# Kernel tuning notes

Measured on AMD Instinct MI355X. Metric: run time of the kernel, lower is better.

## Reference

```python
import jax, jax.numpy as jnp
import numpy as np

N_NODES = 50000
N_EDGES = 600000
K = 4
BN_EPS = 1e-5


def setup_inputs() -> dict:
    key = jax.random.key(0)
    ks = jax.random.split(key, 8)
    x = jax.random.normal(ks[0], (N_NODES, 128), dtype=jnp.float32)
    edge_index = jax.random.randint(ks[1], (2, N_EDGES), 0, N_NODES, dtype=jnp.int64)
    edge_weight = jax.random.uniform(ks[2], (N_EDGES,), dtype=jnp.float32)
    conv_w = jax.random.normal(ks[3], (10, K, 128, 128), dtype=jnp.float32)
    conv_b = jnp.zeros((10, 128), dtype=jnp.float32)
    bn_gamma = jnp.ones((10, 128), dtype=jnp.float32)
    bn_beta = jnp.zeros((10, 128), dtype=jnp.float32)
    lin_w = jax.random.normal(ks[4], (128, 16), dtype=jnp.float32)
    lin_b = jnp.zeros((16,), dtype=jnp.float32)
    return {"x": x, "edge_index": edge_index, "edge_weight": edge_weight,
            "conv_w": conv_w, "conv_b": conv_b, "bn_gamma": bn_gamma,
            "bn_beta": bn_beta, "lin_w": lin_w, "lin_b": lin_b}


def _cheb_norm(edge_index, edge_weight, n_nodes):
    # PyG ChebConv with lambda_max=2, sym normalization:
    # L_hat = 2L/lambda_max - I = -D^{-1/2} A D^{-1/2}, zero diagonal.
    row, col = edge_index[0], edge_index[1]
    w = jnp.where(row == col, 0.0, edge_weight)  # remove_self_loops
    deg = jax.ops.segment_sum(w, row, num_segments=n_nodes)
    dis = jnp.where(deg > 0, jax.lax.rsqrt(jnp.where(deg > 0, deg, 1.0)), 0.0)
    norm = -dis[row] * w * dis[col]
    return norm


def _propagate(h, norm, src, dst, n_nodes):
    # (L_hat h)[i] = sum over edges (src->dst==i) norm_e * h[src_e]
    return jax.ops.segment_sum(norm[:, None] * h[src], dst, num_segments=n_nodes)


def _cheb_conv(h, norm, src, dst, W, b, n_nodes):
    # W: [K, F_in, F_out]; Chebyshev recurrence T0=h, T1=Lh, Tk=2L T_{k-1} - T_{k-2}
    Tx0 = h
    out = Tx0 @ W[0]
    Tx1 = _propagate(Tx0, norm, src, dst, n_nodes)
    out = out + Tx1 @ W[1]
    for k in range(2, W.shape[0]):
        Tx2 = 2.0 * _propagate(Tx1, norm, src, dst, n_nodes) - Tx0
        out = out + Tx2 @ W[k]
        Tx0, Tx1 = Tx1, Tx2
    return out + b


def _batchnorm(h, gamma, beta):
    mean = jnp.mean(h, axis=0)
    var = jnp.mean(jnp.square(h - mean), axis=0)  # biased, as torch BN
    return gamma * (h - mean) * jax.lax.rsqrt(var + BN_EPS) + beta


def reference(x, edge_index, edge_weight, conv_w, conv_b, bn_gamma, bn_beta, lin_w, lin_b):
    n_nodes = x.shape[0]
    src, dst = edge_index[0], edge_index[1]
    norm = _cheb_norm(edge_index, edge_weight, n_nodes)
    h = x
    for i in range(10):
        h = jax.nn.relu(_cheb_conv(h, norm, src, dst, conv_w[i], conv_b[i], n_nodes))
        h = _batchnorm(h, bn_gamma[i], bn_beta[i])
        # dropout: identity (eval mode / deterministic reference)
    return h @ lin_w + lin_b
```

## Files before the change

### kernel.cpp

```cpp
#include <hip/hip_runtime.h>
#include <hip/hip_bf16.h>
#include <cstddef>

#define NN 50000
#define NE 600000
#define FD 128
#define NL 10
#define BN_EPS 1e-5f
#define NBG ((NN + 127) / 128)
#define SCB ((NN + 255) / 256)

typedef _Float16 f16x8 __attribute__((ext_vector_type(8)));
typedef _Float16 f16x2 __attribute__((ext_vector_type(2)));
typedef float f32x4 __attribute__((ext_vector_type(4)));

__global__ void k_detect(const unsigned int* __restrict__ gamma_raw,
                         const unsigned int* __restrict__ idx_raw,
                         int* __restrict__ flags) {
  if (threadIdx.x == 0 && blockIdx.x == 0) {
    flags[0] = (gamma_raw[0] == 0x3F803F80u) ? 1 : 0;
    int i64 = 1;
    for (int i = 1; i < 64; i += 2)
      if (idx_raw[i] != 0u) i64 = 0;
    flags[1] = i64;
  }
}

__device__ __forceinline__ float ld_f(const void* src, int i, int isbf) {
  if (isbf) {
    unsigned int u = ((const unsigned short*)src)[i];
    return __uint_as_float(u << 16);
  }
  return ((const float*)src)[i];
}

#define R_IDX 1200000
#define R_H   4400000
#define R_EW  5000000
#define R_W   5655360
#define R_P   5661392
__global__ void k_pre(const void* __restrict__ x, const void* __restrict__ eidx,
                      const void* __restrict__ ew, const void* __restrict__ convw,
                      const void* __restrict__ convb, const void* __restrict__ gamma,
                      const void* __restrict__ beta, const void* __restrict__ linw,
                      const void* __restrict__ linb,
                      int* __restrict__ idx32, unsigned int* __restrict__ hbuf,
                      float* __restrict__ ewf, unsigned short* __restrict__ wt,
                      float* __restrict__ convbf, float* __restrict__ gammaf,
                      float* __restrict__ betaf, float* __restrict__ linwf,
                      float* __restrict__ linbf, float* __restrict__ stid,
                      const int* __restrict__ flags) {
  int gid = blockIdx.x * 256 + threadIdx.x;
  int isbf = flags[0];
  if (gid < R_IDX) {
    if (flags[1]) idx32[gid] = (int)((const long long*)eidx)[gid];
    else          idx32[gid] = ((const int*)eidx)[gid];
  } else if (gid < R_H) {
    int i = gid - R_IDX;
    f16x2 p;
    p.x = (_Float16)ld_f(x, i * 2, isbf);
    p.y = (_Float16)ld_f(x, i * 2 + 1, isbf);
    hbuf[i] = *(unsigned int*)&p;
  } else if (gid < R_EW) {
    int i = gid - R_H;
    ewf[i] = ld_f(ew, i, isbf);
  } else if (gid < R_W) {
    int tid = gid - R_EW;
    int L = tid >> 16;
    int r16 = tid & 65535;
    int s = r16 >> 12;
    int r = r16 & 4095;
    int n = r >> 5, kk = r & 31;
    int kc = s >> 2, kb = s & 3;
    int krow = kb * 32 + kk;
    int base = (L * 4) * FD * FD;
    float v;
    if (kc == 0)
      v = ld_f(convw, base + (0 * FD + krow) * FD + n, isbf)
        - ld_f(convw, base + (2 * FD + krow) * FD + n, isbf);
    else if (kc == 1)
      v = ld_f(convw, base + (1 * FD + krow) * FD + n, isbf)
        - 3.f * ld_f(convw, base + (3 * FD + krow) * FD + n, isbf);
    else if (kc == 2)
      v = 2.f * ld_f(convw, base + (2 * FD + krow) * FD + n, isbf);
    else
      v = 4.f * ld_f(convw, base + (3 * FD + krow) * FD + n, isbf);
    _Float16 h = (_Float16)v;
    wt[tid] = *(unsigned short*)&h;
  } else if (gid < R_P) {
    int i = gid - R_W;
    if (i < 1280) convbf[i] = ld_f(convb, i, isbf);
    else if (i < 2560) gammaf[i - 1280] = ld_f(gamma, i - 1280, isbf);
    else if (i < 3840) betaf[i - 2560] = ld_f(beta, i - 2560, isbf);
    else if (i < 5888) linwf[i - 3840] = ld_f(linw, i - 3840, isbf);
    else if (i < 5904) linbf[i - 5888] = ld_f(linb, i - 5888, isbf);
    else { int f = i - 5904; stid[f] = 1.f; stid[128 + f] = 0.f; }
  }
}

__global__ void k_deg(const int* __restrict__ src, const int* __restrict__ dst,
                      const float* __restrict__ w, float* __restrict__ deg,
                      int* __restrict__ counts, int m) {
  int e = blockIdx.x * 256 + threadIdx.x;
  if (e >= m) return;
  int s = src[e], d = dst[e];
  float ww = (s == d) ? 0.f : w[e];
  atomicAdd(&deg[s], ww);
  atomicAdd(&counts[d], 1);
}

__global__ void k_dis(float* __restrict__ deg, int n) {
  int i = blockIdx.x * 256 + threadIdx.x;
  if (i >= n) return;
  float d = deg[i];
  deg[i] = (d > 0.f) ? rsqrtf(d) : 0.f;
}

__global__ void k_scan1(const int* __restrict__ counts, int* __restrict__ bsum, int n) {
  __shared__ int sd[256];
  int i = blockIdx.x * 256 + threadIdx.x;
  sd[threadIdx.x] = (i < n) ? counts[i] : 0;
  __syncthreads();
  for (int off = 128; off; off >>= 1) {
    if (threadIdx.x < off) sd[threadIdx.x] += sd[threadIdx.x + off];
    __syncthreads();
  }
  if (threadIdx.x == 0) bsum[blockIdx.x] = sd[0];
}

__global__ void k_scan2(const int* __restrict__ bsum, int* __restrict__ boff, int nb) {
  __shared__ int sd[256];
  int t = threadIdx.x;
  int v = (t < nb) ? bsum[t] : 0;
  sd[t] = v;
  __syncthreads();
  for (int off = 1; off < 256; off <<= 1) {
    int x = sd[t];
    int add = (t >= off) ? sd[t - off] : 0;
    __syncthreads();
    sd[t] = x + add;
    __syncthreads();
  }
  if (t < nb) boff[t] = sd[t] - v;
}

__global__ void k_scan3(const int* __restrict__ counts, const int* __restrict__ boff,
                        int* __restrict__ rowptr, int* __restrict__ cursor, int n, int m) {
  __shared__ int sd[256];
  int t = threadIdx.x;
  int i = blockIdx.x * 256 + t;
  int v = (i < n) ? counts[i] : 0;
  sd[t] = v;
  __syncthreads();
  for (int off = 1; off < 256; off <<= 1) {
    int x = sd[t];
    int add = (t >= off) ? sd[t - off] : 0;
    __syncthreads();
    sd[t] = x + add;
    __syncthreads();
  }
  if (i < n) {
    int excl = boff[blockIdx.x] + sd[t] - v;
    rowptr[i] = excl;
    cursor[i] = excl;
  }
  if (i == n - 1) rowptr[n] = m;
}

__global__ void k_fill(const int* __restrict__ src, const int* __restrict__ dst,
                       const float* __restrict__ w, const float* __restrict__ dis,
                       int* __restrict__ cursor, int2* __restrict__ esw, int m) {
  int e = blockIdx.x * 256 + threadIdx.x;
  if (e >= m) return;
  int s = src[e], d = dst[e];
  float ww = (s == d) ? 0.f : w[e];
  float nv = -dis[s] * ww * dis[d];
  int pos = atomicAdd(&cursor[d], 1);
  esw[pos] = make_int2(s, __float_as_int(nv));
}

__global__ void k_rowsum(const int* __restrict__ rowptr, const int2* __restrict__ esw,
                         float* __restrict__ rowsum, int n) {
  int node = blockIdx.x * 256 + threadIdx.x;
  if (node >= n) return;
  int beg = rowptr[node], end = rowptr[node + 1];
  float s = 0.f;
  for (int e = beg; e < end; e++) s += __int_as_float(esw[e].y);
  rowsum[node] = s;
}

template <int MODE>
__global__ __launch_bounds__(256) void k_prop(const uint4* __restrict__ h128,
                                              const int* __restrict__ rowptr,
                                              const int2* __restrict__ esw,
                                              const float* __restrict__ st,
                                              const float* __restrict__ rowsum,
                                              uint4* __restrict__ out128, int n) {
  int node = blockIdx.x * 16 + (threadIdx.x >> 4);
  int l = threadIdx.x & 15;
  if (node >= n) return;
  int beg = rowptr[node], end = rowptr[node + 1];
  float a[8];
#pragma unroll
  for (int i = 0; i < 8; i++) a[i] = 0.f;
  for (int e = beg; e < end; e += 8) {
    int   s_[8];
    float w_[8];
#pragma unroll
    for (int j = 0; j < 8; j++) {
      int ee = e + j;
      int ec = (ee < end) ? ee : (end - 1);
      int2 m = esw[ec];
      s_[j] = m.x;
      w_[j] = (ee < end) ? __int_as_float(m.y) : 0.f;
    }
    uint4 g[8];
#pragma unroll
    for (int j = 0; j < 8; j++) g[j] = h128[(size_t)s_[j] * 16 + l];
#pragma unroll
    for (int j = 0; j < 8; j++) {
      f16x2 u0 = *(f16x2*)&g[j].x;
      f16x2 u1 = *(f16x2*)&g[j].y;
      f16x2 u2 = *(f16x2*)&g[j].z;
      f16x2 u3 = *(f16x2*)&g[j].w;
      a[0] = fmaf(w_[j], (float)u0.x, a[0]);
      a[1] = fmaf(w_[j], (float)u0.y, a[1]);
      a[2] = fmaf(w_[j], (float)u1.x, a[2]);
      a[3] = fmaf(w_[j], (float)u1.y, a[3]);
      a[4] = fmaf(w_[j], (float)u2.x, a[4]);
      a[5] = fmaf(w_[j], (float)u2.y, a[5]);
      a[6] = fmaf(w_[j], (float)u3.x, a[6]);
      a[7] = fmaf(w_[j], (float)u3.y, a[7]);
    }
  }
  if (MODE == 0) {
    float4 s0 = *(const float4*)&st[l * 8];
    float4 s1 = *(const float4*)&st[l * 8 + 4];
    float4 t0 = *(const float4*)&st[128 + l * 8];
    float4 t1 = *(const float4*)&st[128 + l * 8 + 4];
    float rs = rowsum[node];
    a[0] = s0.x * a[0] + t0.x * rs;  a[1] = s0.y * a[1] + t0.y * rs;
    a[2] = s0.z * a[2] + t0.z * rs;  a[3] = s0.w * a[3] + t0.w * rs;
    a[4] = s1.x * a[4] + t1.x * rs;  a[5] = s1.y * a[5] + t1.y * rs;
    a[6] = s1.z * a[6] + t1.z * rs;  a[7] = s1.w * a[7] + t1.w * rs;
  }
  f16x2 o0, o1, o2, o3;
  o0.x = (_Float16)a[0]; o0.y = (_Float16)a[1];
  o1.x = (_Float16)a[2]; o1.y = (_Float16)a[3];
  o2.x = (_Float16)a[4]; o2.y = (_Float16)a[5];
  o3.x = (_Float16)a[6]; o3.y = (_Float16)a[7];
  uint4 o;
  o.x = *(unsigned int*)&o0; o.y = *(unsigned int*)&o1;
  o.z = *(unsigned int*)&o2; o.w = *(unsigned int*)&o3;
  out128[(size_t)node * 16 + l] = o;
}

__global__ __launch_bounds__(256) void k_gemm(const unsigned short* __restrict__ T0h,
                                              const unsigned short* __restrict__ T1h,
                                              const unsigned short* __restrict__ T2h,
                                              const unsigned short* __restrict__ T3h,
                                              const unsigned short* __restrict__ Wt,
                                              const float* __restrict__ bias,
                                              const float* __restrict__ st,
                                              unsigned short* __restrict__ outh,
                                              float* __restrict__ stats, int n) {
  __shared__ unsigned short ldsB[2][128 * 40];
  __shared__ float lps[4][128], lqs[4][128];
  int tid = threadIdx.x;
  int wid = tid >> 6, lane = tid & 63;
  int ln = lane & 15, kg = lane >> 4;
  int r0 = blockIdx.x * 128 + wid * 32;

  f32x4 acc[2][8];
#pragma unroll
  for (int rb = 0; rb < 2; rb++)
#pragma unroll
    for (int nb = 0; nb < 8; nb++) acc[rb][nb] = (f32x4){0.f, 0.f, 0.f, 0.f};

  {
    const uint4* g = (const uint4*)(Wt);
    uint4 a = g[tid], b = g[tid + 256];
    *(uint4*)&ldsB[0][(tid >> 2) * 40 + (tid & 3) * 8] = a;
    *(uint4*)&ldsB[0][((tid >> 2) + 64) * 40 + (tid & 3) * 8] = b;
  }
  __syncthreads();

  int rowA0 = r0 + ln;       if (rowA0 >= n) rowA0 = n - 1;
  int rowA1 = r0 + 16 + ln;  if (rowA1 >= n) rowA1 = n - 1;

#pragma unroll
  for (int kc = 0; kc < 4; ++kc) {
    const unsigned short* T = (kc == 0) ? T0h : (kc == 1) ? T1h : (kc == 2) ? T2h : T3h;
#pragma unroll
    for (int kb = 0; kb < 4; ++kb) {
      const int s = kc * 4 + kb;
      const int cur = s & 1;
      uint4 st0, st1;
      if (s < 15) {
        const uint4* g = (const uint4*)(Wt + (s + 1) * 4096);
        st0 = g[tid]; st1 = g[tid + 256];
      }
      f16x8 a0 = *(const f16x8*)(T + (size_t)rowA0 * FD + kb * 32 + kg * 8);
      f16x8 a1 = *(const f16x8*)(T + (size_t)rowA1 * FD + kb * 32 + kg * 8);
      if (kc == 0) {
        const float* sb = st + kb * 32 + kg * 8;
        const float* tb = st + 128 + kb * 32 + kg * 8;
#pragma unroll
        for (int j = 0; j < 8; j++) {
          a0[j] = (_Float16)(sb[j] * (float)a0[j] + tb[j]);
          a1[j] = (_Float16)(sb[j] * (float)a1[j] + tb[j]);
        }
      }
      f16x8 bf[8];
#pragma unroll
      for (int nb = 0; nb < 8; nb++)
        bf[nb] = *(const f16x8*)&ldsB[cur][(nb * 16 + ln) * 40 + kg * 8];
#pragma unroll
      for (int nb = 0; nb < 8; nb++) {
        acc[0][nb] = __builtin_amdgcn_mfma_f32_16x16x32_f16(a0, bf[nb], acc[0][nb], 0, 0, 0);
        acc[1][nb] = __builtin_amdgcn_mfma_f32_16x16x32_f16(a1, bf[nb], acc[1][nb], 0, 0, 0);
      }
      if (s < 15) {
        *(uint4*)&ldsB[cur ^ 1][(tid >> 2) * 40 + (tid & 3) * 8] = st0;
        *(uint4*)&ldsB[cur ^ 1][((tid >> 2) + 64) * 40 + (tid & 3) * 8] = st1;
      }
      __syncthreads();
    }
  }

  float psum[8], psq[8];
#pragma unroll
  for (int nb = 0; nb < 8; nb++) { psum[nb] = 0.f; psq[nb] = 0.f; }
#pragma unroll
  for (int rb = 0; rb < 2; rb++) {
#pragma unroll
    for (int nb = 0; nb < 8; nb++) {
      int col = nb * 16 + ln;
      float bs = bias[col];
#pragma unroll
      for (int r = 0; r < 4; r++) {
        int row = r0 + rb * 16 + kg * 4 + r;
        if (row < n) {
          float v = acc[rb][nb][r] + bs;
          v = fmaxf(v, 0.f);
          _Float16 hv = (_Float16)v;
          outh[(size_t)row * FD + col] = *(unsigned short*)&hv;
          psum[nb] += v;
          psq[nb] += v * v;
        }
      }
    }
  }
#pragma unroll
  for (int nb = 0; nb < 8; nb++) {
    float sv = psum[nb], qv = psq[nb];
    sv += __shfl_xor(sv, 16); sv += __shfl_xor(sv, 32);
    qv += __shfl_xor(qv, 16); qv += __shfl_xor(qv, 32);
    if (kg == 0) { lps[wid][nb * 16 + ln] = sv; lqs[wid][nb * 16 + ln] = qv; }
  }
  __syncthreads();
  if (tid < 128) {
    float sv = lps[0][tid] + lps[1][tid] + lps[2][tid] + lps[3][tid];
    atomicAdd(&stats[tid], sv);
  } else {
    int c = tid - 128;
    float qv = lqs[0][c] + lqs[1][c] + lqs[2][c] + lqs[3][c];
    atomicAdd(&stats[128 + c], qv);
  }
}

__global__ void k_bnfin(const float* __restrict__ stats,
                        const float* __restrict__ gamma, const float* __restrict__ beta,
                        float* __restrict__ st, float invN) {
  int f = threadIdx.x;
  float mean = stats[f] * invN;
  float var = stats[128 + f] * invN - mean * mean;
  float sc = gamma[f] * rsqrtf(var + BN_EPS);
  st[f] = sc;
  st[128 + f] = beta[f] - mean * sc;
}

__global__ void k_final(const unsigned short* __restrict__ h, const float* __restrict__ w,
                        const float* __restrict__ b, const float* __restrict__ st,
                        void* __restrict__ out, int n, const int* __restrict__ flags) {
  __shared__ float lw[2048];
  __shared__ float ls[128], lt[128];
  for (int i = threadIdx.x; i < 2048; i += 256) lw[i] = w[i];
  if (threadIdx.x < 128) { ls[threadIdx.x] = st[threadIdx.x]; lt[threadIdx.x] = st[128 + threadIdx.x]; }
  __syncthreads();
  int node = blockIdx.x * 256 + threadIdx.x;
  if (node >= n) return;
  float acc[16];
#pragma unroll
  for (int c = 0; c < 16; c++) acc[c] = b[c];
  const f16x8* hr = (const f16x8*)(h + (size_t)node * FD);
#pragma unroll 2
  for (int k8 = 0; k8 < 16; k8++) {
    f16x8 hv = hr[k8];
#pragma unroll
    for (int j = 0; j < 8; j++) {
      int f = k8 * 8 + j;
      float x = ls[f] * (float)hv[j] + lt[f];
#pragma unroll
      for (int c = 0; c < 16; c++) acc[c] = fmaf(x, lw[f * 16 + c], acc[c]);
    }
  }
  int isbf = flags[0];
  for (int c = 0; c < 16; c++) {
    int idx = node * 16 + c;
    if (isbf) ((__hip_bfloat16*)out)[idx] = __float2bfloat16(acc[c]);
    else      ((float*)out)[idx] = acc[c];
  }
}

extern "C" void kernel_launch(void* const* d_in, const int* in_sizes, int n_in,
                              void* d_out, int out_size, void* d_ws, size_t ws_size,
                              hipStream_t stream) {
  char* p = (char*)d_ws;
  auto take = [&](size_t bytes) -> void* {
    void* r = (void*)p;
    p += (bytes + 255) & ~size_t(255);
    return r;
  };
  int*   flags  = (int*)  take(64);
  int*   idx32  = (int*)  take(sizeof(int) * 2 * NE);
  float* ewf    = (float*)take(sizeof(float) * NE);
  unsigned short* wtws = (unsigned short*)take(sizeof(short) * NL * 16 * 4096);
  float* convbf = (float*)take(sizeof(float) * NL * FD);
  float* gammaf = (float*)take(sizeof(float) * NL * FD);
  float* betaf  = (float*)take(sizeof(float) * NL * FD);
  float* linwf  = (float*)take(sizeof(float) * FD * 16);
  float* linbf  = (float*)take(sizeof(float) * 16);
  char*  zb     = (char*) take(sizeof(float) * NN + sizeof(int) * NN + sizeof(float) * NL * 256);
  float* deg    = (float*)zb;
  int*   counts = (int*)  (zb + sizeof(float) * NN);
  float* stats  = (float*)(zb + sizeof(float) * NN + sizeof(int) * NN);
  float* rowsum = (float*)take(sizeof(float) * NN);
  int*   rowptr = (int*)  take(sizeof(int) * (NN + 1));
  int*   cursor = (int*)  take(sizeof(int) * NN);
  int*   bsum   = (int*)  take(sizeof(int) * SCB);
  int*   boff   = (int*)  take(sizeof(int) * SCB);
  int2*  esw    = (int2*) take(sizeof(int2) * NE);
  unsigned int* hbuf = (unsigned int*)take(sizeof(int) * (size_t)NN * 64);
  unsigned int* t1   = (unsigned int*)take(sizeof(int) * (size_t)NN * 64);
  unsigned int* t2   = (unsigned int*)take(sizeof(int) * (size_t)NN * 64);
  unsigned int* t3   = (unsigned int*)take(sizeof(int) * (size_t)NN * 64);
  float* stcur  = (float*)take(sizeof(float) * 256);
  float* stid   = (float*)take(sizeof(float) * 256);

  k_detect<<<1, 64, 0, stream>>>((const unsigned int*)d_in[5], (const unsigned int*)d_in[1], flags);

  k_pre<<<(R_P + 255) / 256, 256, 0, stream>>>(d_in[0], d_in[1], d_in[2], d_in[3], d_in[4],
                                               d_in[5], d_in[6], d_in[7], d_in[8],
                                               idx32, hbuf, ewf, wtws,
                                               convbf, gammaf, betaf, linwf, linbf, stid, flags);

  hipMemsetAsync(zb, 0, sizeof(float) * NN + sizeof(int) * NN + sizeof(float) * NL * 256, stream);

  const int* srcI = idx32;
  const int* dstI = idx32 + NE;
  k_deg<<<(NE + 255) / 256, 256, 0, stream>>>(srcI, dstI, ewf, deg, counts, NE);
  k_dis<<<(NN + 255) / 256, 256, 0, stream>>>(deg, NN);
  k_scan1<<<SCB, 256, 0, stream>>>(counts, bsum, NN);
  k_scan2<<<1, 256, 0, stream>>>(bsum, boff, SCB);
  k_scan3<<<SCB, 256, 0, stream>>>(counts, boff, rowptr, cursor, NN, NE);
  k_fill<<<(NE + 255) / 256, 256, 0, stream>>>(srcI, dstI, ewf, deg, cursor, esw, NE);
  k_rowsum<<<(NN + 255) / 256, 256, 0, stream>>>(rowptr, esw, rowsum, NN);

  for (int L = 0; L < NL; ++L) {
    const unsigned short* Wt = wtws + (size_t)L * 16 * 4096;
    const float* stIn = (L == 0) ? stid : stcur;
    k_prop<0><<<(NN + 15) / 16, 256, 0, stream>>>((const uint4*)hbuf, rowptr, esw, stIn, rowsum, (uint4*)t1, NN);
    k_prop<1><<<(NN + 15) / 16, 256, 0, stream>>>((const uint4*)t1, rowptr, esw, nullptr, nullptr, (uint4*)t2, NN);
    k_prop<1><<<(NN + 15) / 16, 256, 0, stream>>>((const uint4*)t2, rowptr, esw, nullptr, nullptr, (uint4*)t3, NN);
    k_gemm<<<NBG, 256, 0, stream>>>((const unsigned short*)hbuf, (const unsigned short*)t1,
                                    (const unsigned short*)t2, (const unsigned short*)t3,
                                    Wt, convbf + L * FD, stIn, (unsigned short*)hbuf, stats + L * 256, NN);
    k_bnfin<<<1, 128, 0, stream>>>(stats + L * 256, gammaf + L * FD, betaf + L * FD, stcur, 1.0f / NN);
  }

  k_final<<<(NN + 255) / 256, 256, 0, stream>>>((const unsigned short*)hbuf, linwf, linbf, stcur, d_out, NN, flags);
}
```

Measured before the change: 1.172 ms.

## Pack edges into 32-bit words, sort nodes by degree bucket, fold BN finalize

Each CSR edge entry shrinks from an int2 to one 32-bit word holding a 16-bit source index and an fp16 normalized weight, halving edge-stream traffic in the propagation kernels. A degree-bucketing pass builds a node order that groups nodes of similar degree so 16-lane groups in a block do similar amounts of gather work. The batch-norm finalize kernel is removed: prop, gemm and final now compute scale and shift from the raw stats in shared memory. The separate rsqrt-degree kernel is fused into the first scan kernel. The cost is reduced precision on edge weights, a 65535-node limit on the packed index, and one extra indirection per node through the order array.

```diff
diff --git a/kernel.cpp b/kernel.cpp
--- a/kernel.cpp
+++ b/kernel.cpp
@@ -9,6 +9,7 @@
 #define BN_EPS 1e-5f
 #define NBG ((NN + 127) / 128)
 #define SCB ((NN + 255) / 256)
+#define NBK 9
 
 typedef _Float16 f16x8 __attribute__((ext_vector_type(8)));
 typedef _Float16 f16x2 __attribute__((ext_vector_type(2)));
@@ -38,7 +39,7 @@
 #define R_H   4400000
 #define R_EW  5000000
 #define R_W   5655360
-#define R_P   5661392
+#define R_P   5661312
 __global__ void k_pre(const void* __restrict__ x, const void* __restrict__ eidx,
                       const void* __restrict__ ew, const void* __restrict__ convw,
                       const void* __restrict__ convb, const void* __restrict__ gamma,
@@ -48,7 +49,7 @@
                       float* __restrict__ ewf, unsigned short* __restrict__ wt,
                       float* __restrict__ convbf, float* __restrict__ gammaf,
                       float* __restrict__ betaf, float* __restrict__ linwf,
-                      float* __restrict__ linbf, float* __restrict__ stid,
+                      float* __restrict__ linbf,
                       const int* __restrict__ flags) {
   int gid = blockIdx.x * 256 + threadIdx.x;
   int isbf = flags[0];
@@ -94,7 +95,6 @@
     else if (i < 3840) betaf[i - 2560] = ld_f(beta, i - 2560, isbf);
     else if (i < 5888) linwf[i - 3840] = ld_f(linw, i - 3840, isbf);
     else if (i < 5904) linbf[i - 5888] = ld_f(linb, i - 5888, isbf);
-    else { int f = i - 5904; stid[f] = 1.f; stid[128 + f] = 0.f; }
   }
 }
 
@@ -109,16 +109,14 @@
   atomicAdd(&counts[d], 1);
 }
 
-__global__ void k_dis(float* __restrict__ deg, int n) {
-  int i = blockIdx.x * 256 + threadIdx.x;
-  if (i >= n) return;
-  float d = deg[i];
-  deg[i] = (d > 0.f) ? rsqrtf(d) : 0.f;
-}
-
-__global__ void k_scan1(const int* __restrict__ counts, int* __restrict__ bsum, int n) {
+__global__ void k_dis_scan1(float* __restrict__ deg, const int* __restrict__ counts,
+                            int* __restrict__ bsum, int n) {
   __shared__ int sd[256];
   int i = blockIdx.x * 256 + threadIdx.x;
+  if (i < n) {
+    float d = deg[i];
+    deg[i] = (d > 0.f) ? rsqrtf(d) : 0.f;
+  }
   sd[threadIdx.x] = (i < n) ? counts[i] : 0;
   __syncthreads();
   for (int off = 128; off; off >>= 1) {
@@ -169,36 +167,93 @@
 
 __global__ void k_fill(const int* __restrict__ src, const int* __restrict__ dst,
                        const float* __restrict__ w, const float* __restrict__ dis,
-                       int* __restrict__ cursor, int2* __restrict__ esw, int m) {
+                       int* __restrict__ cursor, unsigned int* __restrict__ esw, int m) {
   int e = blockIdx.x * 256 + threadIdx.x;
   if (e >= m) return;
   int s = src[e], d = dst[e];
   float ww = (s == d) ? 0.f : w[e];
   float nv = -dis[s] * ww * dis[d];
+  _Float16 hv = (_Float16)nv;
+  unsigned int pk = (unsigned int)s | ((unsigned int)*(unsigned short*)&hv << 16);
   int pos = atomicAdd(&cursor[d], 1);
-  esw[pos] = make_int2(s, __float_as_int(nv));
-}
-
-__global__ void k_rowsum(const int* __restrict__ rowptr, const int2* __restrict__ esw,
-                         float* __restrict__ rowsum, int n) {
-  int node = blockIdx.x * 256 + threadIdx.x;
-  if (node >= n) return;
-  int beg = rowptr[node], end = rowptr[node + 1];
-  float s = 0.f;
-  for (int e = beg; e < end; e++) s += __int_as_float(esw[e].y);
-  rowsum[node] = s;
+  esw[pos] = pk;
+}
+
+__global__ void k_rowsum(const int* __restrict__ rowptr, const unsigned int* __restrict__ esw,
+                         float* __restrict__ rowsum, int* __restrict__ bcount, int n) {
+  __shared__ int lcnt[NBK];
+  int t = threadIdx.x;
+  if (t < NBK) lcnt[t] = 0;
+  __syncthreads();
+  int node = blockIdx.x * 256 + t;
+  if (node < n) {
+    int beg = rowptr[node], end = rowptr[node + 1];
+    float s = 0.f;
+    for (int e = beg; e < end; e++) {
+      unsigned short hw = (unsigned short)(esw[e] >> 16);
+      s += (float)*(_Float16*)&hw;
+    }
+    rowsum[node] = s;
+    int b = (end - beg + 7) >> 3; if (b > 8) b = 8;
+    atomicAdd(&lcnt[b], 1);
+  }
+  __syncthreads();
+  if (t < NBK && lcnt[t]) atomicAdd(&bcount[t], lcnt[t]);
+}
+
+__global__ void k_border(const int* __restrict__ rowptr, const int* __restrict__ bcount,
+                         int* __restrict__ bcur, int* __restrict__ order, int n) {
+  __shared__ int lcnt[NBK], lbase[NBK], sboff[NBK];
+  int t = threadIdx.x;
+  if (t < NBK) lcnt[t] = 0;
+  if (t == 0) {
+    int run = 0;
+    for (int i = 0; i < NBK; i++) { sboff[i] = run; run += bcount[i]; }
+  }
+  __syncthreads();
+  int node = blockIdx.x * 256 + t;
+  int b = 0, my = 0;
+  if (node < n) {
+    int cn = rowptr[node + 1] - rowptr[node];
+    b = (cn + 7) >> 3; if (b > 8) b = 8;
+    my = atomicAdd(&lcnt[b], 1);
+  }
+  __syncthreads();
+  if (t < NBK) lbase[t] = lcnt[t] ? atomicAdd(&bcur[t], lcnt[t]) : 0;
+  __syncthreads();
+  if (node < n) order[sboff[b] + lbase[b] + my] = node;
 }
 
 template <int MODE>
 __global__ __launch_bounds__(256) void k_prop(const uint4* __restrict__ h128,
+                                              const int* __restrict__ order,
                                               const int* __restrict__ rowptr,
-                                              const int2* __restrict__ esw,
-                                              const float* __restrict__ st,
+                                              const unsigned int* __restrict__ esw,
+                                              const float* __restrict__ stats,
+                                              const float* __restrict__ gamma,
+                                              const float* __restrict__ beta,
                                               const float* __restrict__ rowsum,
-                                              uint4* __restrict__ out128, int n) {
-  int node = blockIdx.x * 16 + (threadIdx.x >> 4);
-  int l = threadIdx.x & 15;
-  if (node >= n) return;
+                                              uint4* __restrict__ out128,
+                                              float invN, int n) {
+  __shared__ float ls[128], lt[128];
+  int tid = threadIdx.x;
+  if (MODE == 0) {
+    if (tid < 128) {
+      float s, t;
+      if (stats) {
+        float mean = stats[tid] * invN;
+        float var = stats[128 + tid] * invN - mean * mean;
+        s = gamma[tid] * rsqrtf(var + BN_EPS);
+        t = beta[tid] - mean * s;
+      } else { s = 1.f; t = 0.f; }
+      ls[tid] = s; lt[tid] = t;
+    }
+    __syncthreads();
+  }
+  int idx = blockIdx.x * 16 + (tid >> 4);
+  int l = tid & 15;
+  if (idx >= n) return;
+  int node = order[idx];
   int beg = rowptr[node], end = rowptr[node + 1];
   float a[8];
 #pragma unroll
@@ -210,9 +265,10 @@
     for (int j = 0; j < 8; j++) {
       int ee = e + j;
       int ec = (ee < end) ? ee : (end - 1);
-      int2 m = esw[ec];
-      s_[j] = m.x;
-      w_[j] = (ee < end) ? __int_as_float(m.y) : 0.f;
+      unsigned int m = esw[ec];
+      s_[j] = m & 0xFFFFu;
+      unsigned short hw = (unsigned short)(m >> 16);
+      w_[j] = (ee < end) ? (float)*(_Float16*)&hw : 0.f;
     }
     uint4 g[8];
 #pragma unroll
@@ -234,15 +290,9 @@
     }
   }
   if (MODE == 0) {
-    float4 s0 = *(const float4*)&st[l * 8];
-    float4 s1 = *(const float4*)&st[l * 8 + 4];
-    float4 t0 = *(const float4*)&st[128 + l * 8];
-    float4 t1 = *(const float4*)&st[128 + l * 8 + 4];
     float rs = rowsum[node];
-    a[0] = s0.x * a[0] + t0.x * rs;  a[1] = s0.y * a[1] + t0.y * rs;
-    a[2] = s0.z * a[2] + t0.z * rs;  a[3] = s0.w * a[3] + t0.w * rs;
-    a[4] = s1.x * a[4] + t1.x * rs;  a[5] = s1.y * a[5] + t1.y * rs;
-    a[6] = s1.z * a[6] + t1.z * rs;  a[7] = s1.w * a[7] + t1.w * rs;
+#pragma unroll
+    for (int j = 0; j < 8; j++) a[j] = ls[l * 8 + j] * a[j] + lt[l * 8 + j] * rs;
   }
   f16x2 o0, o1, o2, o3;
   o0.x = (_Float16)a[0]; o0.y = (_Float16)a[1];
@@ -261,15 +311,30 @@
                                               const unsigned short* __restrict__ T3h,
                                               const unsigned short* __restrict__ Wt,
                                               const float* __restrict__ bias,
-                                              const float* __restrict__ st,
+                                              const float* __restrict__ statsPrev,
+                                              const float* __restrict__ gamma,
+                                              const float* __restrict__ beta,
                                               unsigned short* __restrict__ outh,
-                                              float* __restrict__ stats, int n) {
+                                              float* __restrict__ stats,
+                                              float invN, int n) {
   __shared__ unsigned short ldsB[2][128 * 40];
   __shared__ float lps[4][128], lqs[4][128];
+  __shared__ float ls[128], lt[128];
   int tid = threadIdx.x;
   int wid = tid >> 6, lane = tid & 63;
   int ln = lane & 15, kg = lane >> 4;
   int r0 = blockIdx.x * 128 + wid * 32;
+
+  if (tid < 128) {
+    float s, t;
+    if (statsPrev) {
+      float mean = statsPrev[tid] * invN;
+      float var = statsPrev[128 + tid] * invN - mean * mean;
+      s = gamma[tid] * rsqrtf(var + BN_EPS);
+      t = beta[tid] - mean * s;
+    } else { s = 1.f; t = 0.f; }
+    ls[tid] = s; lt[tid] = t;
+  }
 
   f32x4 acc[2][8];
 #pragma unroll
@@ -303,12 +368,11 @@
       f16x8 a0 = *(const f16x8*)(T + (size_t)rowA0 * FD + kb * 32 + kg * 8);
       f16x8 a1 = *(const f16x8*)(T + (size_t)rowA1 * FD + kb * 32 + kg * 8);
       if (kc == 0) {
-        const float* sb = st + kb * 32 + kg * 8;
-        const float* tb = st + 128 + kb * 32 + kg * 8;
 #pragma unroll
         for (int j = 0; j < 8; j++) {
-          a0[j] = (_Float16)(sb[j] * (float)a0[j] + tb[j]);
-          a1[j] = (_Float16)(sb[j] * (float)a1[j] + tb[j]);
+          int f = kb * 32 + kg * 8 + j;
+          a0[j] = (_Float16)(ls[f] * (float)a0[j] + lt[f]);
+          a1[j] = (_Float16)(ls[f] * (float)a1[j] + lt[f]);
         }
       }
       f16x8 bf[8];
@@ -369,24 +433,22 @@
   }
 }
 
-__global__ void k_bnfin(const float* __restrict__ stats,
+__global__ void k_final(const unsigned short* __restrict__ h, const float* __restrict__ w,
+                        const float* __restrict__ b, const float* __restrict__ stats,
                         const float* __restrict__ gamma, const float* __restrict__ beta,
-                        float* __restrict__ st, float invN) {
-  int f = threadIdx.x;
-  float mean = stats[f] * invN;
-  float var = stats[128 + f] * invN - mean * mean;
-  float sc = gamma[f] * rsqrtf(var + BN_EPS);
-  st[f] = sc;
-  st[128 + f] = beta[f] - mean * sc;
-}
-
-__global__ void k_final(const unsigned short* __restrict__ h, const float* __restrict__ w,
-                        const float* __restrict__ b, const float* __restrict__ st,
-                        void* __restrict__ out, int n, const int* __restrict__ flags) {
+                        void* __restrict__ out, float invN, int n,
+                        const int* __restrict__ flags) {
   __shared__ float lw[2048];
   __shared__ float ls[128], lt[128];
   for (int i = threadIdx.x; i < 2048; i += 256) lw[i] = w[i];
-  if (threadIdx.x < 128) { ls[threadIdx.x] = st[threadIdx.x]; lt[threadIdx.x] = st[128 + threadIdx.x]; }
+  if (threadIdx.x < 128) {
+    int f = threadIdx.x;
+    float mean = stats[f] * invN;
+    float var = stats[128 + f] * invN - mean * mean;
+    float s = gamma[f] * rsqrtf(var + BN_EPS);
+    ls[f] = s;
+    lt[f] = beta[f] - mean * s;
+  }
   __syncthreads();
   int node = blockIdx.x * 256 + threadIdx.x;
   if (node >= n) return;
@@ -431,53 +493,65 @@
   float* betaf  = (float*)take(sizeof(float) * NL * FD);
   float* linwf  = (float*)take(sizeof(float) * FD * 16);
   float* linbf  = (float*)take(sizeof(float) * 16);
-  char*  zb     = (char*) take(sizeof(float) * NN + sizeof(int) * NN + sizeof(float) * NL * 256);
+  size_t zbsz   = sizeof(float) * NN + sizeof(int) * NN + sizeof(float) * NL * 256 + 128;
+  char*  zb     = (char*) take(zbsz);
   float* deg    = (float*)zb;
   int*   counts = (int*)  (zb + sizeof(float) * NN);
   float* stats  = (float*)(zb + sizeof(float) * NN + sizeof(int) * NN);
+  int*   bcount = (int*)  (zb + sizeof(float) * NN + sizeof(int) * NN + sizeof(float) * NL * 256);
+  int*   bcur   = bcount + 16;
   float* rowsum = (float*)take(sizeof(float) * NN);
   int*   rowptr = (int*)  take(sizeof(int) * (NN + 1));
   int*   cursor = (int*)  take(sizeof(int) * NN);
   int*   bsum   = (int*)  take(sizeof(int) * SCB);
   int*   boff   = (int*)  take(sizeof(int) * SCB);
-  int2*  esw    = (int2*) take(sizeof(int2) * NE);
+  int*   order  = (int*)  take(sizeof(int) * NN);
+  unsigned int* esw = (unsigned int*)take(sizeof(int) * NE);
   unsigned int* hbuf = (unsigned int*)take(sizeof(int) * (size_t)NN * 64);
   unsigned int* t1   = (unsigned int*)take(sizeof(int) * (size_t)NN * 64);
   unsigned int* t2   = (unsigned int*)take(sizeof(int) * (size_t)NN * 64);
   unsigned int* t3   = (unsigned int*)take(sizeof(int) * (size_t)NN * 64);
-  float* stcur  = (float*)take(sizeof(float) * 256);
-  float* stid   = (float*)take(sizeof(float) * 256);
 
   k_detect<<<1, 64, 0, stream>>>((const unsigned int*)d_in[5], (const unsigned int*)d_in[1], flags);
 
   k_pre<<<(R_P + 255) / 256, 256, 0, stream>>>(d_in[0], d_in[1], d_in[2], d_in[3], d_in[4],
                                                d_in[5], d_in[6], d_in[7], d_in[8],
                                                idx32, hbuf, ewf, wtws,
-                                               convbf, gammaf, betaf, linwf, linbf, stid, flags);
-
-  hipMemsetAsync(zb, 0, sizeof(float) * NN + sizeof(int) * NN + sizeof(float) * NL * 256, stream);
+                                               convbf, gammaf, betaf, linwf, linbf, flags);
+
+  hipMemsetAsync(zb, 0, zbsz, stream);
 
   const int* srcI = idx32;
   const int* dstI = idx32 + NE;
   k_deg<<<(NE + 255) / 256, 256, 0, stream>>>(srcI, dstI, ewf, deg, counts, NE);
-  k_dis<<<(NN + 255) / 256, 256, 0, stream>>>(deg, NN);
-  k_scan1<<<SCB, 256, 0, stream>>>(counts, bsum, NN);
+  k_dis_scan1<<<SCB, 256, 0, stream>>>(deg, counts, bsum, NN);
   k_scan2<<<1, 256, 0, stream>>>(bsum, boff, SCB);
   k_scan3<<<SCB, 256, 0, stream>>>(counts, boff, rowptr, cursor, NN, NE);
   k_fill<<<(NE + 255) / 256, 256, 0, stream>>>(srcI, dstI, ewf, deg, cursor, esw, NE);
-  k_rowsum<<<(NN + 255) / 256, 256, 0, stream>>>(rowptr, esw, rowsum, NN);
-
+  k_rowsum<<<SCB, 256, 0, stream>>>(rowptr, esw, rowsum, bcount, NN);
+  k_border<<<SCB, 256, 0, stream>>>(rowptr, bcount, bcur, order, NN);
+
+  const float invN = 1.0f / NN;
   for (int L = 0; L < NL; ++L) {
     const unsigned short* Wt = wtws + (size_t)L * 16 * 4096;
-    const float* stIn = (L == 0) ? stid : stcur;
-    k_prop<0><<<(NN + 15) / 16, 256, 0, stream>>>((const uint4*)hbuf, rowptr, esw, stIn, rowsum, (uint4*)t1, NN);
-    k_prop<1><<<(NN + 15) / 16, 256, 0, stream>>>((const uint4*)t1, rowptr, esw, nullptr, nullptr, (uint4*)t2, NN);
-    k_prop<1><<<(NN + 15) / 16, 256, 0, stream>>>((const uint4*)t2, rowptr, esw, nullptr, nullptr, (uint4*)t3, NN);
+    const float* sPrev = (L == 0) ? nullptr : stats + (size_t)(L - 1) * 256;
+    const float* gPrev = gammaf + (size_t)(L ? L - 1 : 0) * FD;
+    const float* bPrev = betaf + (size_t)(L ? L - 1 : 0) * FD;
+    k_prop<0><<<(NN + 15) / 16, 256, 0, stream>>>((const uint4*)hbuf, order, rowptr, esw,
+                                                  sPrev, gPrev, bPrev, rowsum, (uint4*)t1, invN, NN);
+    k_prop<1><<<(NN + 15) / 16, 256, 0, stream>>>((const uint4*)t1, order, rowptr, esw,
+                                                  nullptr, nullptr, nullptr, nullptr, (uint4*)t2, invN, NN);
+    k_prop<1><<<(NN + 15) / 16, 256, 0, stream>>>((const uint4*)t2, order, rowptr, esw,
+                                                  nullptr, nullptr, nullptr, nullptr, (uint4*)t3, invN, NN);
     k_gemm<<<NBG, 256, 0, stream>>>((const unsigned short*)hbuf, (const unsigned short*)t1,
                                     (const unsigned short*)t2, (const unsigned short*)t3,
-                                    Wt, convbf + L * FD, stIn, (unsigned short*)hbuf, stats + L * 256, NN);
-    k_bnfin<<<1, 128, 0, stream>>>(stats + L * 256, gammaf + L * FD, betaf + L * FD, stcur, 1.0f / NN);
-  }
-
-  k_final<<<(NN + 255) / 256, 256, 0, stream>>>((const unsigned short*)hbuf, linwf, linbf, stcur, d_out, NN, flags);
-}
+                                    Wt, convbf + L * FD, sPrev, gPrev, bPrev,
+                                    (unsigned short*)hbuf, stats + (size_t)L * 256, invN, NN);
+  }
+
+  k_final<<<(NN + 255) / 256, 256, 0, stream>>>((const unsigned short*)hbuf, linwf, linbf,
+                                                stats + (size_t)(NL - 1) * 256,
+                                                gammaf + (size_t)(NL - 1) * FD,
+                                                betaf + (size_t)(NL - 1) * FD,
+                                                d_out, invN, NN, flags);
+}
```

Result: faster. 1.131 ms (-3.5%).
